# Optimization experiments

Hardware: AMD Instinct MI355X
Metric: run time of the kernel (lower is better)

The kernel has to match this reference:

```python
import jax, jax.numpy as jnp
import numpy as np

EMBED_DIM = 128
NUM_SYMBOLS = 200000
PAD_IDX = NUM_SYMBOLS
K_NEIGHBORS = 10
PROCESS_STEPS = 4
D_MODEL = 2 * EMBED_DIM   # 256
D_INNER = 2 * D_MODEL     # 512
LSTM_HID = 2 * D_MODEL    # 512
B, F_SUP, MAX_K = 4096, 5, 64


def setup_inputs() -> dict:
    key = jax.random.key(0)
    ks = jax.random.split(key, 40)
    f = lambda i, shape, s=0.05: jax.random.normal(ks[i], shape, jnp.float32) * s
    inp = {}
    inp['query'] = jax.random.randint(ks[0], (B, 2), 0, NUM_SYMBOLS)
    inp['support'] = jax.random.randint(ks[1], (F_SUP, 2), 0, NUM_SYMBOLS)
    inp['q_l1'] = jax.random.randint(ks[2], (B, MAX_K, 2), 0, NUM_SYMBOLS + 1)
    inp['q_deg_l'] = jax.random.randint(ks[3], (B,), 0, 100)
    inp['q_r1'] = jax.random.randint(ks[4], (B, MAX_K, 2), 0, NUM_SYMBOLS + 1)
    inp['q_deg_r'] = jax.random.randint(ks[5], (B,), 0, 100)
    inp['s_l1'] = jax.random.randint(ks[6], (F_SUP, MAX_K, 2), 0, NUM_SYMBOLS + 1)
    inp['s_deg_l'] = jax.random.randint(ks[7], (F_SUP,), 0, 100)
    inp['s_r1'] = jax.random.randint(ks[8], (F_SUP, MAX_K, 2), 0, NUM_SYMBOLS + 1)
    inp['s_deg_r'] = jax.random.randint(ks[9], (F_SUP,), 0, 100)
    # learned parameters
    inp['symbol_emb'] = f(10, (NUM_SYMBOLS + 1, EMBED_DIM), 0.1).at[PAD_IDX].set(0.0)
    inp['gcn_w_w'] = f(11, (EMBED_DIM, 2 * EMBED_DIM))
    inp['gcn_w_b'] = jnp.zeros((EMBED_DIM,), jnp.float32)
    inp['gcn_b'] = jnp.zeros((EMBED_DIM,), jnp.float32)
    inp['g1_w'] = f(12, (EMBED_DIM // 2, EMBED_DIM))
    inp['g1_b'] = jnp.zeros((EMBED_DIM // 2,), jnp.float32)
    inp['ln1_g'] = jnp.ones((EMBED_DIM // 2,), jnp.float32)
    inp['ln1_b'] = jnp.zeros((EMBED_DIM // 2,), jnp.float32)
    inp['g2_w'] = f(13, (1, EMBED_DIM // 2))
    inp['g2_b'] = jnp.zeros((1,), jnp.float32)
    inp['gate_temp'] = jnp.array(1.0, jnp.float32)
    inp['se_p1_w'] = f(14, (D_INNER, D_MODEL))
    inp['se_p1_b'] = jnp.zeros((D_INNER,), jnp.float32)
    inp['se_p2_w'] = f(15, (D_MODEL, D_INNER))
    inp['se_p2_b'] = jnp.zeros((D_MODEL,), jnp.float32)
    inp['se_ln_g'] = jnp.ones((D_MODEL,), jnp.float32)
    inp['se_ln_b'] = jnp.zeros((D_MODEL,), jnp.float32)
    inp['w_ih'] = f(16, (4 * LSTM_HID, D_MODEL))
    inp['w_hh'] = f(17, (4 * LSTM_HID, LSTM_HID))
    inp['b_ih'] = jnp.zeros((4 * LSTM_HID,), jnp.float32)
    inp['b_hh'] = jnp.zeros((4 * LSTM_HID,), jnp.float32)
    return inp


def _layernorm(x, g, b, eps=1e-5):
    m = jnp.mean(x, axis=-1, keepdims=True)
    v = jnp.var(x, axis=-1, keepdims=True)
    return (x - m) / jnp.sqrt(v + eps) * g + b


def _l2norm(x):
    return x / jnp.maximum(jnp.linalg.norm(x, axis=-1, keepdims=True), 1e-12)


def _neighbor_encoder(conn, deg, self_ids, p):
    emb = p['symbol_emb']
    rel, ent = conn[:, :, 0], conn[:, :, 1]
    rel_emb = emb[rel]            # [n, K, D] gather
    ent_emb = emb[ent]            # [n, K, D]
    self_emb = emb[self_ids]      # [n, D]
    sim = jnp.einsum('nd,nkd->nk', _l2norm(self_emb), _l2norm(ent_emb))
    is_pad = (rel == PAD_IDX).astype(jnp.float32)
    sim = sim - is_pad * 1e9
    k = min(K_NEIGHBORS, conn.shape[1])
    _, k_idx = jax.lax.top_k(sim, k)
    bidx = jnp.arange(conn.shape[0])[:, None]
    k_mask = jnp.zeros(sim.shape, jnp.float32).at[bidx, k_idx].set(1.0)[..., None]
    concat = jnp.concatenate([rel_emb, ent_emb], axis=-1)   # [n, K, 2D]
    proj = jax.nn.leaky_relu(concat @ p['gcn_w_w'].T + p['gcn_w_b'] + p['gcn_b'], 0.01)
    valid = (1.0 - is_pad[..., None]) * k_mask
    denom = jnp.maximum(jnp.sum(valid, axis=1), 1.0)
    agg = jnp.sum((proj * k_mask) * valid, axis=1) / denom   # [n, D]
    h = jax.nn.relu(_layernorm(agg @ p['g1_w'].T + p['g1_b'], p['ln1_g'], p['ln1_b']))
    logit = h @ p['g2_w'].T + p['g2_b']                      # [n, 1]
    temp = jnp.clip(p['gate_temp'], 0.1, 5.0)
    gate = jax.nn.sigmoid(logit / temp) * (deg > 0).astype(jnp.float32)[:, None]
    return jnp.tanh(self_emb + gate * agg)


def _support_encoder(x, p):
    h = jax.nn.relu(x @ p['se_p1_w'].T + p['se_p1_b'])
    h = h @ p['se_p2_w'].T + p['se_p2_b']
    return _layernorm(h + x, p['se_ln_g'], p['se_ln_b'])


def _query_encoder(support, query, p):
    n = query.shape[0]
    h_r0 = jnp.zeros((n, LSTM_HID), jnp.float32)
    c0 = jnp.zeros((n, LSTM_HID), jnp.float32)

    def step(carry, _):
        h_r, c = carry
        gates = query @ p['w_ih'].T + p['b_ih'] + h_r @ p['w_hh'].T + p['b_hh']
        i, f, g, o = jnp.split(gates, 4, axis=-1)
        c = jax.nn.sigmoid(f) * c + jax.nn.sigmoid(i) * jnp.tanh(g)
        h_ = jax.nn.sigmoid(o) * jnp.tanh(c)
        h = query + h_[:, :D_MODEL]
        attn = jax.nn.softmax(h @ support.T, axis=1)
        r = attn @ support
        return (jnp.concatenate([h, r], axis=-1), c), None

    (h_r, _), _ = jax.lax.scan(step, (h_r0, c0), None, length=PROCESS_STEPS)
    return h_r[:, :D_MODEL]


def reference(query, support, q_l1, q_deg_l, q_r1, q_deg_r, s_l1, s_deg_l, s_r1, s_deg_r,
              symbol_emb, gcn_w_w, gcn_w_b, gcn_b, g1_w, g1_b, ln1_g, ln1_b, g2_w, g2_b,
              gate_temp, se_p1_w, se_p1_b, se_p2_w, se_p2_b, se_ln_g, se_ln_b,
              w_ih, w_hh, b_ih, b_hh):
    p = dict(symbol_emb=symbol_emb, gcn_w_w=gcn_w_w, gcn_w_b=gcn_w_b, gcn_b=gcn_b,
             g1_w=g1_w, g1_b=g1_b, ln1_g=ln1_g, ln1_b=ln1_b, g2_w=g2_w, g2_b=g2_b,
             gate_temp=gate_temp, se_p1_w=se_p1_w, se_p1_b=se_p1_b, se_p2_w=se_p2_w,
             se_p2_b=se_p2_b, se_ln_g=se_ln_g, se_ln_b=se_ln_b,
             w_ih=w_ih, w_hh=w_hh, b_ih=b_ih, b_hh=b_hh)
    q_left = _neighbor_encoder(q_l1, q_deg_l, query[:, 0], p)
    q_right = _neighbor_encoder(q_r1, q_deg_r, query[:, 1], p)
    query_vec = jnp.concatenate([q_left, q_right], axis=-1)      # [B, 2D]
    s_left = _neighbor_encoder(s_l1, s_deg_l, support[:, 0], p)
    s_right = _neighbor_encoder(s_r1, s_deg_r, support[:, 1], p)
    support_vec = jnp.concatenate([s_left, s_right], axis=-1)    # [F, 2D]
    support_g = jnp.mean(_support_encoder(support_vec, p), axis=0, keepdims=True)  # [1, 2D]
    query_enc = _support_encoder(query_vec, p)                   # [B, 2D]
    query_g = _query_encoder(support_g, query_enc, p)            # [B, 2D]
    return jnp.sum(query_g * support_g, axis=1)                  # [B]
```

## Files before the change

kernel.cpp:

```cpp
#include <hip/hip_runtime.h>
#include <math.h>

#define BQ 4096
#define F_SUP 5
#define MAXK 64
#define ED 128
#define DM 256
#define DI 512
#define LH 512
#define NG 2048
#define PADX 200000
#define KNB 10
#define MROWS 82048
#define MREAL 82020
#define MQ 4224

typedef unsigned short u16;
typedef __attribute__((ext_vector_type(8))) short short8;
typedef __attribute__((ext_vector_type(4))) float floatx4;

__device__ __forceinline__ float sigf(float x) { return 1.0f / (1.0f + __expf(-x)); }
__device__ __forceinline__ float tanh_fast(float x) {
  float a = fabsf(x);
  float e = __expf(-2.0f * a);
  float t = (1.0f - e) / (1.0f + e);
  return copysignf(t, x);
}
__device__ __forceinline__ u16 f2bf(float f) {
  unsigned u = __float_as_uint(f);
  unsigned r = (u + 0x7FFFu + ((u >> 16) & 1u)) >> 16;
  return (u16)r;
}
__device__ __forceinline__ float bf2f(u16 u) {
  return __uint_as_float(((unsigned)u) << 16);
}
__device__ __forceinline__ void gl2lds16(const void* g, void* l) {
  __builtin_amdgcn_global_load_lds(
      (const __attribute__((address_space(1))) void*)g,
      (__attribute__((address_space(3))) void*)l, 16, 0, 0);
}

__global__ __launch_bounds__(256) void nbr_sim_kernel(
    const int* __restrict__ query, const int* __restrict__ support,
    const int* __restrict__ q_l1, const int* __restrict__ q_r1,
    const int* __restrict__ s_l1, const int* __restrict__ s_r1,
    const float* __restrict__ emb, float* __restrict__ simG)
{
  __shared__ __align__(16) float sE[128];
  int tid = threadIdx.x;
  int b = blockIdx.x;
  const int* conn; int self_id;
  if (b < BQ)              { int i = b;              conn = q_l1 + (long)i*(MAXK*2); self_id = query[2*i];   }
  else if (b < 2*BQ)       { int i = b - BQ;         conn = q_r1 + (long)i*(MAXK*2); self_id = query[2*i+1]; }
  else if (b < 2*BQ+F_SUP) { int i = b - 2*BQ;       conn = s_l1 + (long)i*(MAXK*2); self_id = support[2*i]; }
  else                     { int i = b - 2*BQ-F_SUP; conn = s_r1 + (long)i*(MAXK*2); self_id = support[2*i+1]; }

  int k = tid >> 2, part = tid & 3;
  int2 rc = *(const int2*)(conn + 2 * k);
  if (tid < 32) *(float4*)&sE[tid * 4] = *(const float4*)(emb + (long)self_id * ED + tid * 4);
  __syncthreads();

  const float* er = emb + (long)rc.y * ED + part * 4;
  float dot = 0.f, sq = 0.f;
  #pragma unroll
  for (int i = 0; i < 8; ++i) {
    float4 e = *(const float4*)(er + i * 16);
    float4 s = *(const float4*)(&sE[i * 16 + part * 4]);
    dot += e.x*s.x + e.y*s.y + e.z*s.z + e.w*s.w;
    sq  += e.x*e.x + e.y*e.y + e.z*e.z + e.w*e.w;
  }
  dot += __shfl_xor(dot, 1); dot += __shfl_xor(dot, 2);
  sq  += __shfl_xor(sq, 1);  sq  += __shfl_xor(sq, 2);
  if (part == 0) {
    float ne = fmaxf(sqrtf(sq), 1e-12f);
    float sim = dot / ne;
    if (rc.x == PADX) sim -= 1e9f;
    simG[(long)b * 64 + k] = sim;
  }
}

__global__ __launch_bounds__(256) void nbr_rank_kernel(
    const int* __restrict__ q_l1, const int* __restrict__ q_r1,
    const int* __restrict__ s_l1, const int* __restrict__ s_r1,
    const float* __restrict__ simG, int* __restrict__ idxA, int* __restrict__ meta)
{
  int tid = threadIdx.x;
  int wave = tid >> 6, lane = tid & 63;
  int b = blockIdx.x * 4 + wave;
  if (b < 2 * BQ + 2 * F_SUP) {
    const int* conn;
    if (b < BQ)              conn = q_l1 + (long)b * (MAXK*2);
    else if (b < 2*BQ)       conn = q_r1 + (long)(b - BQ) * (MAXK*2);
    else if (b < 2*BQ+F_SUP) conn = s_l1 + (long)(b - 2*BQ) * (MAXK*2);
    else                     conn = s_r1 + (long)(b - 2*BQ - F_SUP) * (MAXK*2);

    float my = simG[(long)b * 64 + lane];
    int rank = 0;
    #pragma unroll
    for (int j = 0; j < 64; ++j) {
      float s = __shfl(my, j);
      rank += ((s > my) || (s == my && j < lane)) ? 1 : 0;
    }
    int2 rc = *(const int2*)(conn + 2 * lane);
    bool val = (rank < KNB) && (rc.x != PADX);
    unsigned long long vm = __ballot(val ? 1 : 0);
    int cnt = __popcll(vm);
    long base = (long)b * 10;
    if (val) {
      int pos = __popcll(vm & ((1ull << lane) - 1ull));
      *(int2*)(idxA + (base + pos) * 2) = rc;
    }
    if (lane >= cnt && lane < KNB) {
      int2 pp; pp.x = PADX; pp.y = PADX;
      *(int2*)(idxA + (base + lane) * 2) = pp;
    }
    if (lane == 0) meta[b] = cnt;
  }
  if (blockIdx.x == 0 && tid < 2 * (MROWS - MREAL)) {
    idxA[(long)MREAL * 2 + tid] = PADX;
  }
}

__global__ __launch_bounds__(256) void proj_gather_gemm(
    const int* __restrict__ idxA, const float* __restrict__ emb,
    const u16* __restrict__ W, u16* __restrict__ proj)
{
  __shared__ u16 As[128 * 32];
  __shared__ u16 Bs[128 * 32];
  __shared__ int idxS[256];
  int tid = threadIdx.x;
  int bm = blockIdx.x;
  idxS[tid] = idxA[bm * 256 + tid];
  int lane = tid & 63, wave = tid >> 6;
  int wm = (wave & 1) * 64, wn = (wave >> 1) * 64;
  int col = lane & 15, quad = lane >> 4;
  int r = tid >> 1, part = tid & 1;

  floatx4 acc[4][4];
  #pragma unroll
  for (int i = 0; i < 4; ++i)
    #pragma unroll
    for (int j = 0; j < 4; ++j) { floatx4 z = {0.f,0.f,0.f,0.f}; acc[i][j] = z; }
  __syncthreads();

  for (int k0 = 0; k0 < 256; k0 += 32) {
    int half = k0 >> 7, koff = k0 & 127;
    #pragma unroll
    for (int t = 0; t < 2; ++t) {
      int c = t * 256 + tid;
      int rb = c >> 2, o = c & 3;
      int og = o ^ (rb & 3);
      gl2lds16(W + (long)rb * 256 + k0 + og * 8, &Bs[(size_t)c * 8]);
    }
    {
      int id = idxS[r * 2 + half];
      const float* src = emb + (long)id * ED + koff + part * 16;
      float4 f0 = *(const float4*)(src);
      float4 f1 = *(const float4*)(src + 4);
      float4 f2 = *(const float4*)(src + 8);
      float4 f3 = *(const float4*)(src + 12);
      short8 s0, s1;
      s0[0]=(short)f2bf(f0.x); s0[1]=(short)f2bf(f0.y); s0[2]=(short)f2bf(f0.z); s0[3]=(short)f2bf(f0.w);
      s0[4]=(short)f2bf(f1.x); s0[5]=(short)f2bf(f1.y); s0[6]=(short)f2bf(f1.z); s0[7]=(short)f2bf(f1.w);
      s1[0]=(short)f2bf(f2.x); s1[1]=(short)f2bf(f2.y); s1[2]=(short)f2bf(f2.z); s1[3]=(short)f2bf(f2.w);
      s1[4]=(short)f2bf(f3.x); s1[5]=(short)f2bf(f3.y); s1[6]=(short)f2bf(f3.z); s1[7]=(short)f2bf(f3.w);
      int o0 = 2 * part, o1 = 2 * part + 1;
      *(short8*)&As[(size_t)(r * 4 + (o0 ^ (r & 3))) * 8] = s0;
      *(short8*)&As[(size_t)(r * 4 + (o1 ^ (r & 3))) * 8] = s1;
    }
    __syncthreads();
    short8 af[4], bfr[4];
    #pragma unroll
    for (int i = 0; i < 4; ++i) {
      int ra = wm + i * 16 + col;
      af[i] = *(const short8*)&As[(size_t)(ra * 4 + (quad ^ (ra & 3))) * 8];
      int rb = wn + i * 16 + col;
      bfr[i] = *(const short8*)&Bs[(size_t)(rb * 4 + (quad ^ (rb & 3))) * 8];
    }
    #pragma unroll
    for (int i = 0; i < 4; ++i)
      #pragma unroll
      for (int j = 0; j < 4; ++j)
        acc[i][j] = __builtin_amdgcn_mfma_f32_16x16x32_bf16(af[i], bfr[j], acc[i][j], 0, 0, 0);
    __syncthreads();
  }
  int gm0 = bm * 128 + wm + quad * 4;
  int gn0 = wn + col;
  #pragma unroll
  for (int i = 0; i < 4; ++i)
    #pragma unroll
    for (int j = 0; j < 4; ++j)
      #pragma unroll
      for (int rr = 0; rr < 4; ++rr)
        proj[(long)(gm0 + i * 16 + rr) * 128 + gn0 + j * 16] = f2bf(acc[i][j][rr]);
}

__global__ __launch_bounds__(128) void nbr_post_kernel(
    const int* __restrict__ query, const int* __restrict__ support,
    const int* __restrict__ q_deg_l, const int* __restrict__ q_deg_r,
    const int* __restrict__ s_deg_l, const int* __restrict__ s_deg_r,
    const float* __restrict__ emb,
    const u16* __restrict__ proj, const int* __restrict__ meta,
    const float* __restrict__ gcn_w_b, const float* __restrict__ gcn_b,
    const float* __restrict__ g1_w, const float* __restrict__ g1_b,
    const float* __restrict__ ln1_g, const float* __restrict__ ln1_b,
    const float* __restrict__ g2_w, const float* __restrict__ g2_b,
    const float* __restrict__ gate_temp,
    float* __restrict__ qv, u16* __restrict__ qv_bf)
{
  __shared__ __align__(16) float aggS[128];
  __shared__ float sEs[128];
  __shared__ float gateS;
  int tid = threadIdx.x, b = blockIdx.x;
  int deg, self_id, row, colb;
  if (b < BQ)              { int i = b;              deg = q_deg_l[i]; self_id = query[2*i];     row = i;        colb = 0;  }
  else if (b < 2*BQ)       { int i = b - BQ;         deg = q_deg_r[i]; self_id = query[2*i+1];   row = i;        colb = ED; }
  else if (b < 2*BQ+F_SUP) { int i = b - 2*BQ;       deg = s_deg_l[i]; self_id = support[2*i];   row = BQ + i;   colb = 0;  }
  else                     { int i = b - 2*BQ-F_SUP; deg = s_deg_r[i]; self_id = support[2*i+1]; row = BQ + i;   colb = ED; }
  float* outp = qv + (long)row * DM + colb;
  u16*  outpb = qv_bf + (long)row * DM + colb;

  int cnt = meta[b];
  float denom = fmaxf((float)cnt, 1.0f);
  float bsum = gcn_w_b[tid] + gcn_b[tid];
  float agg = 0.f;
  long pbase = (long)b * 10;
  for (int kk = 0; kk < cnt; ++kk) {
    float z = bf2f(proj[(pbase + kk) * 128 + tid]) + bsum;
    z = (z >= 0.f) ? z : 0.01f * z;
    agg += z;
  }
  agg /= denom;
  aggS[tid] = agg;
  sEs[tid] = emb[(long)self_id * ED + tid];
  __syncthreads();

  if (tid < 64) {
    int e = tid;
    const float4* g1r = (const float4*)(g1_w + e * ED);
    float y = g1_b[e];
    #pragma unroll 8
    for (int j = 0; j < 32; ++j) {
      float4 w = g1r[j];
      float4 a = *(const float4*)&aggS[j * 4];
      y += w.x*a.x + w.y*a.y + w.z*a.z + w.w*a.w;
    }
    float s = y;
    #pragma unroll
    for (int off = 1; off < 64; off <<= 1) s += __shfl_xor(s, off);
    float mean = s * (1.0f / 64.0f);
    float dv = y - mean;
    float s2 = dv * dv;
    #pragma unroll
    for (int off = 1; off < 64; off <<= 1) s2 += __shfl_xor(s2, off);
    float var = s2 * (1.0f / 64.0f);
    float hv = dv / sqrtf(var + 1e-5f) * ln1_g[e] + ln1_b[e];
    hv = fmaxf(hv, 0.f);
    float lp = hv * g2_w[e];
    #pragma unroll
    for (int off = 1; off < 64; off <<= 1) lp += __shfl_xor(lp, off);
    if (e == 0) {
      float logit = lp + g2_b[0];
      float temp = fminf(fmaxf(gate_temp[0], 0.1f), 5.0f);
      float gate = 1.0f / (1.0f + expf(-logit / temp));
      if (deg <= 0) gate = 0.f;
      gateS = gate;
    }
  }
  __syncthreads();
  float o = tanhf(sEs[tid] + gateS * aggS[tid]);
  outp[tid] = o;
  outpb[tid] = f2bf(o);
}

__global__ __launch_bounds__(256) void mfma_gemm(
    const u16* __restrict__ A, int lda,
    const u16* __restrict__ W, int ldw,
    int N, int K,
    float* __restrict__ Cout, u16* __restrict__ Cbf,
    const float* __restrict__ bias0,
    const u16* __restrict__ gqin,
    u16* __restrict__ gqout,
    int relu, int lstm_mode,
    float* __restrict__ cstate, const float* __restrict__ qe,
    u16* __restrict__ hbf)
{
  __shared__ u16 As[128 * 32];
  __shared__ u16 Bs[128 * 32];
  int tid = threadIdx.x;
  int nb = N >> 7;
  int bn = blockIdx.x % nb, bm = blockIdx.x / nb;
  int lane = tid & 63, wave = tid >> 6;
  int wm = (wave & 1) * 64, wn = (wave >> 1) * 64;
  int col = lane & 15, quad = lane >> 4;

  u16 gqa[64]; float cpv[16]; float qev[16]; float scv[4];
  int u = 0; long fb = 0;
  if (lstm_mode) {
    u = bn * 32 + (wave >> 1) * 16 + col;
    fb = ((long)blockIdx.x * 4 + wave) * 64 + lane;
    #pragma unroll
    for (int j = 0; j < 4; ++j)
      scv[j] = bias0[bn * 128 + (wave >> 1) * 64 + j * 16 + col];
    if (lstm_mode == 1) {
      const short8* gp = (const short8*)(gqin + fb * 64);
      #pragma unroll
      for (int t = 0; t < 8; ++t) *(short8*)&gqa[t * 8] = gp[t];
      const float4* cp = (const float4*)(cstate + fb * 16);
      #pragma unroll
      for (int t = 0; t < 4; ++t) *(float4*)&cpv[t * 4] = cp[t];
    }
    if (u < DM) {
      #pragma unroll
      for (int i = 0; i < 4; ++i)
        #pragma unroll
        for (int r = 0; r < 4; ++r) {
          int m = bm * 128 + (wave & 1) * 64 + i * 16 + quad * 4 + r;
          qev[i * 4 + r] = qe[(long)m * DM + u];
        }
    }
  }

  floatx4 acc[4][4];
  #pragma unroll
  for (int i = 0; i < 4; ++i)
    #pragma unroll
    for (int j = 0; j < 4; ++j) { floatx4 z = {0.f,0.f,0.f,0.f}; acc[i][j] = z; }

  for (int k0 = 0; k0 < K; k0 += 32) {
    #pragma unroll
    for (int t = 0; t < 2; ++t) {
      int c = t * 256 + tid;
      int r = c >> 2, o = c & 3;
      int og = o ^ (r & 3);
      gl2lds16(A + (long)(bm * 128 + r) * lda + k0 + og * 8, &As[(size_t)c * 8]);
      gl2lds16(W + (long)(bn * 128 + r) * ldw + k0 + og * 8, &Bs[(size_t)c * 8]);
    }
    __syncthreads();
    short8 af[4], bfr[4];
    #pragma unroll
    for (int i = 0; i < 4; ++i) {
      int ra = wm + i * 16 + col;
      af[i] = *(const short8*)&As[(size_t)(ra * 4 + (quad ^ (ra & 3))) * 8];
      int rb = wn + i * 16 + col;
      bfr[i] = *(const short8*)&Bs[(size_t)(rb * 4 + (quad ^ (rb & 3))) * 8];
    }
    #pragma unroll
    for (int i = 0; i < 4; ++i)
      #pragma unroll
      for (int j = 0; j < 4; ++j)
        acc[i][j] = __builtin_amdgcn_mfma_f32_16x16x32_bf16(af[i], bfr[j], acc[i][j], 0, 0, 0);
    __syncthreads();
  }

  if (lstm_mode) {
    float cnew[16];
    #pragma unroll
    for (int i = 0; i < 4; ++i) {
      #pragma unroll
      for (int r = 0; r < 4; ++r) {
        float gI = acc[i][0][r] + scv[0];
        float gF = acc[i][1][r] + scv[1];
        float gG = acc[i][2][r] + scv[2];
        float gO = acc[i][3][r] + scv[3];
        if (lstm_mode == 1) {
          gI += bf2f(gqa[(i * 4 + 0) * 4 + r]);
          gF += bf2f(gqa[(i * 4 + 1) * 4 + r]);
          gG += bf2f(gqa[(i * 4 + 2) * 4 + r]);
          gO += bf2f(gqa[(i * 4 + 3) * 4 + r]);
        }
        float cp = (lstm_mode == 2) ? 0.f : cpv[i * 4 + r];
        float cn = sigf(gF) * cp + sigf(gI) * tanh_fast(gG);
        cnew[i * 4 + r] = cn;
        if (u < DM) {
          int m = bm * 128 + (wave & 1) * 64 + i * 16 + quad * 4 + r;
          hbf[(long)m * DM + u] = f2bf(qev[i * 4 + r] + sigf(gO) * tanh_fast(cn));
        }
      }
    }
    {
      float4* cp = (float4*)(cstate + fb * 16);
      #pragma unroll
      for (int t = 0; t < 4; ++t) cp[t] = *(float4*)&cnew[t * 4];
    }
    if (lstm_mode == 2) {
      u16 ga[64];
      #pragma unroll
      for (int i = 0; i < 4; ++i)
        #pragma unroll
        for (int j = 0; j < 4; ++j)
          #pragma unroll
          for (int r = 0; r < 4; ++r)
            ga[(i * 4 + j) * 4 + r] = f2bf(acc[i][j][r] + scv[j]);
      short8* gp = (short8*)(gqout + fb * 64);
      #pragma unroll
      for (int t = 0; t < 8; ++t) gp[t] = *(short8*)&ga[t * 8];
    }
  } else {
    int gm0 = bm * 128 + wm + quad * 4;
    int gn0 = bn * 128 + wn + col;
    #pragma unroll
    for (int i = 0; i < 4; ++i) {
      #pragma unroll
      for (int j = 0; j < 4; ++j) {
        int n = gn0 + j * 16;
        #pragma unroll
        for (int r = 0; r < 4; ++r) {
          int m = gm0 + i * 16 + r;
          float v = acc[i][j][r];
          if (bias0) v += bias0[n];
          if (relu) v = fmaxf(v, 0.f);
          if (Cout) Cout[(long)m * N + n] = v;
          if (Cbf)  Cbf[(long)m * N + n] = f2bf(v);
        }
      }
    }
  }
}

__global__ void prep_cast(
    const float* __restrict__ p1, const float* __restrict__ p2,
    const float* __restrict__ gcnw, const float* __restrict__ wih,
    const float* __restrict__ whh, const float* __restrict__ bih,
    const float* __restrict__ bhh,
    u16* __restrict__ p1b, u16* __restrict__ p2b, u16* __restrict__ gcnb,
    u16* __restrict__ wihb, u16* __restrict__ whhb, float* __restrict__ bihh)
{
  int gid = blockIdx.x * 256 + threadIdx.x;
  if (gid < 131072) { p1b[gid] = f2bf(p1[gid]); }
  else if (gid < 262144) { int i = gid - 131072; p2b[i] = f2bf(p2[i]); }
  else if (gid < 294912) { int i = gid - 262144; gcnb[i] = f2bf(gcnw[i]); }
  else if (gid < 819200) {
    int i = gid - 294912; int p = i >> 8, k = i & 255;
    int g = (p >> 4) & 3, uu = (p >> 7) * 32 + ((p >> 6) & 1) * 16 + (p & 15);
    int n = g * 512 + uu;
    wihb[i] = f2bf(wih[(long)n * DM + k]);
  } else if (gid < 1343488) {
    int i = gid - 819200; int p = i >> 8, k = i & 255;
    int g = (p >> 4) & 3, uu = (p >> 7) * 32 + ((p >> 6) & 1) * 16 + (p & 15);
    int n = g * 512 + uu;
    whhb[i] = f2bf(whh[(long)n * LH + k]);
  } else if (gid < 1345536) {
    int p = gid - 1343488;
    int g = (p >> 4) & 3, uu = (p >> 7) * 32 + ((p >> 6) & 1) * 16 + (p & 15);
    int n = g * 512 + uu;
    bihh[p] = bih[n] + bhh[n];
  }
}

__global__ __launch_bounds__(256) void ln_residual_kernel(
    const float* __restrict__ h2buf, const float* __restrict__ xbuf,
    const float* __restrict__ lng, const float* __restrict__ lnb,
    float* __restrict__ out, u16* __restrict__ outb)
{
  __shared__ float red[4];
  int r = blockIdx.x, tid = threadIdx.x;
  float v = h2buf[(long)r * DM + tid] + xbuf[(long)r * DM + tid];
  float s = v;
  #pragma unroll
  for (int off = 1; off < 64; off <<= 1) s += __shfl_xor(s, off);
  if ((tid & 63) == 0) red[tid >> 6] = s;
  __syncthreads();
  float mean = (red[0] + red[1] + red[2] + red[3]) * (1.0f / 256.0f);
  __syncthreads();
  float dv = v - mean;
  float s2 = dv * dv;
  #pragma unroll
  for (int off = 1; off < 64; off <<= 1) s2 += __shfl_xor(s2, off);
  if ((tid & 63) == 0) red[tid >> 6] = s2;
  __syncthreads();
  float var = (red[0] + red[1] + red[2] + red[3]) * (1.0f / 256.0f);
  float o = dv / sqrtf(var + 1e-5f) * lng[tid] + lnb[tid];
  out[(long)r * DM + tid] = o;
  outb[(long)r * DM + tid] = f2bf(o);
}

__global__ __launch_bounds__(256) void scorr_kernel(
    const float* __restrict__ qe, const float* __restrict__ whh,
    float* __restrict__ sg, float* __restrict__ s_corr_perm)
{
  __shared__ float sgS[DM];
  int tid = threadIdx.x;
  {
    float v = 0.f;
    #pragma unroll
    for (int r = 0; r < F_SUP; ++r) v += qe[(long)(BQ + r) * DM + tid];
    v *= (1.0f / (float)F_SUP);
    sgS[tid] = v;
    if (blockIdx.x == 0) sg[tid] = v;
  }
  __syncthreads();
  int wave = tid >> 6, lane = tid & 63;
  int n = blockIdx.x * 4 + wave;
  float4 w = *(const float4*)(whh + (long)n * LH + DM + lane * 4);
  float4 s = *(const float4*)&sgS[lane * 4];
  float d = w.x*s.x + w.y*s.y + w.z*s.z + w.w*s.w;
  #pragma unroll
  for (int off = 1; off < 64; off <<= 1) d += __shfl_xor(d, off);
  if (lane == 0) {
    int g = n >> 9, uu = n & 511;
    int p = (uu >> 5) * 128 + ((uu >> 4) & 1) * 64 + g * 16 + (uu & 15);
    s_corr_perm[p] = d;
  }
}

__global__ __launch_bounds__(256) void final_dot_kernel(
    const u16* __restrict__ h, const float* __restrict__ sg, float* __restrict__ out)
{
  __shared__ float red[4];
  int m = blockIdx.x, tid = threadIdx.x;
  float v = bf2f(h[(long)m * DM + tid]) * sg[tid];
  #pragma unroll
  for (int off = 1; off < 64; off <<= 1) v += __shfl_xor(v, off);
  if ((tid & 63) == 0) red[tid >> 6] = v;
  __syncthreads();
  if (tid == 0) out[m] = red[0] + red[1] + red[2] + red[3];
}

extern "C" void kernel_launch(void* const* d_in, const int* in_sizes, int n_in,
                              void* d_out, int out_size, void* d_ws, size_t ws_size,
                              hipStream_t stream)
{
  const int*   query    = (const int*)  d_in[0];
  const int*   support  = (const int*)  d_in[1];
  const int*   q_l1     = (const int*)  d_in[2];
  const int*   q_deg_l  = (const int*)  d_in[3];
  const int*   q_r1     = (const int*)  d_in[4];
  const int*   q_deg_r  = (const int*)  d_in[5];
  const int*   s_l1     = (const int*)  d_in[6];
  const int*   s_deg_l  = (const int*)  d_in[7];
  const int*   s_r1     = (const int*)  d_in[8];
  const int*   s_deg_r  = (const int*)  d_in[9];
  const float* symbol_emb = (const float*)d_in[10];
  const float* gcn_w_w  = (const float*)d_in[11];
  const float* gcn_w_b  = (const float*)d_in[12];
  const float* gcn_b    = (const float*)d_in[13];
  const float* g1_w     = (const float*)d_in[14];
  const float* g1_b     = (const float*)d_in[15];
  const float* ln1_g    = (const float*)d_in[16];
  const float* ln1_b    = (const float*)d_in[17];
  const float* g2_w     = (const float*)d_in[18];
  const float* g2_b     = (const float*)d_in[19];
  const float* gate_temp= (const float*)d_in[20];
  const float* se_p1_w  = (const float*)d_in[21];
  const float* se_p1_b  = (const float*)d_in[22];
  const float* se_p2_w  = (const float*)d_in[23];
  const float* se_p2_b  = (const float*)d_in[24];
  const float* se_ln_g  = (const float*)d_in[25];
  const float* se_ln_b  = (const float*)d_in[26];
  const float* w_ih     = (const float*)d_in[27];
  const float* w_hh     = (const float*)d_in[28];
  const float* b_ih     = (const float*)d_in[29];
  const float* b_hh     = (const float*)d_in[30];

  float* ws = (float*)d_ws;
  size_t off = 0;
  float* projF   = ws + off; off += (size_t)MROWS * 128 / 2;
  float* idxF    = ws + off; off += (size_t)MROWS * 2;
  float* qv      = ws + off; off += (size_t)MQ * DM;
  float* qe      = ws + off; off += (size_t)MQ * DM;
  float* qv_bfF  = ws + off; off += (size_t)MQ * DM / 2;
  float* qe_bfF  = ws + off; off += (size_t)MQ * DM / 2;
  float* h1bF    = ws + off; off += (size_t)MQ * DI / 2;
  float* H2      = ws + off; off += (size_t)MQ * DM;
  float* gqbF    = ws + off; off += (size_t)BQ * NG / 2;
  float* cstate  = ws + off; off += (size_t)BQ * LH;
  float* hbf0F   = ws + off; off += (size_t)BQ * DM / 2;
  float* hbf1F   = ws + off; off += (size_t)BQ * DM / 2;
  float* p1bF    = ws + off; off += 131072 / 2;
  float* p2bF    = ws + off; off += 131072 / 2;
  float* gcnbF   = ws + off; off += 32768 / 2;
  float* wihbF   = ws + off; off += 524288 / 2;
  float* whhbF   = ws + off; off += 524288 / 2;
  float* bihh    = ws + off; off += 2048;
  float* sg      = ws + off; off += 256;
  float* s_corr  = ws + off; off += 2048;
  float* metaF   = ws + off; off += 8448;
  float* simF    = ws + off; off += (size_t)8448 * 64;

  u16* proj   = (u16*)projF;
  int* idxA   = (int*)idxF;
  u16* qv_bf  = (u16*)qv_bfF;
  u16* qe_bf  = (u16*)qe_bfF;
  u16* H1_bf  = (u16*)h1bF;
  u16* gq_fr  = (u16*)gqbF;
  u16* hbf0   = (u16*)hbf0F;
  u16* hbf1   = (u16*)hbf1F;
  u16* p1b    = (u16*)p1bF;
  u16* p2b    = (u16*)p2bF;
  u16* gcnb   = (u16*)gcnbF;
  u16* wihb   = (u16*)wihbF;
  u16* whhb   = (u16*)whhbF;
  int* meta   = (int*)metaF;

  prep_cast<<<5256, 256, 0, stream>>>(se_p1_w, se_p2_w, gcn_w_w, w_ih, w_hh, b_ih, b_hh,
                                      p1b, p2b, gcnb, wihb, whhb, bihh);

  nbr_sim_kernel<<<2 * BQ + 2 * F_SUP, 256, 0, stream>>>(
      query, support, q_l1, q_r1, s_l1, s_r1, symbol_emb, simF);

  nbr_rank_kernel<<<(2 * BQ + 2 * F_SUP + 3) / 4, 256, 0, stream>>>(
      q_l1, q_r1, s_l1, s_r1, simF, idxA, meta);

  proj_gather_gemm<<<MROWS / 128, 256, 0, stream>>>(idxA, symbol_emb, gcnb, proj);

  nbr_post_kernel<<<2 * BQ + 2 * F_SUP, 128, 0, stream>>>(
      query, support, q_deg_l, q_deg_r, s_deg_l, s_deg_r, symbol_emb,
      proj, meta, gcn_w_b, gcn_b, g1_w, g1_b, ln1_g, ln1_b, g2_w, g2_b, gate_temp,
      qv, qv_bf);

  mfma_gemm<<<(MQ / 128) * (DI / 128), 256, 0, stream>>>(qv_bf, 256, p1b, 256, DI, 256,
      nullptr, H1_bf, se_p1_b, nullptr, nullptr, 1, 0, nullptr, nullptr, nullptr);
  mfma_gemm<<<(MQ / 128) * (DM / 128), 256, 0, stream>>>(H1_bf, 512, p2b, 512, DM, 512,
      H2, nullptr, se_p2_b, nullptr, nullptr, 0, 0, nullptr, nullptr, nullptr);
  ln_residual_kernel<<<BQ + F_SUP, 256, 0, stream>>>(H2, qv, se_ln_g, se_ln_b, qe, qe_bf);

  scorr_kernel<<<512, 256, 0, stream>>>(qe, w_hh, sg, s_corr);

  mfma_gemm<<<(BQ / 128) * (NG / 128), 256, 0, stream>>>(qe_bf, 256, wihb, 256, NG, 256,
      nullptr, nullptr, bihh, nullptr, gq_fr, 0, 2, cstate, qe, hbf0);

  mfma_gemm<<<(BQ / 128) * (NG / 128), 256, 0, stream>>>(hbf0, 256, whhb, 256, NG, 256,
      nullptr, nullptr, s_corr, gq_fr, nullptr, 0, 1, cstate, qe, hbf1);
  mfma_gemm<<<(BQ / 128) * (NG / 128), 256, 0, stream>>>(hbf1, 256, whhb, 256, NG, 256,
      nullptr, nullptr, s_corr, gq_fr, nullptr, 0, 1, cstate, qe, hbf0);
  mfma_gemm<<<(BQ / 128) * (NG / 128), 256, 0, stream>>>(hbf0, 256, whhb, 256, NG, 256,
      nullptr, nullptr, s_corr, gq_fr, nullptr, 0, 1, cstate, qe, hbf1);

  final_dot_kernel<<<BQ, 256, 0, stream>>>(hbf1, sg, (float*)d_out);
}
```

Measured before the change: 428.1 us.

## Pre-cast embedding table to bf16, fuse sim and rank, gather via LDS loads

Adds a pass that converts the whole embedding table to bf16 each call. The neighbor-similarity and top-k ranking kernels now read the halved-size rows and are merged into one kernel, with ranking done through shared memory. The projection GEMM gathers bf16 embedding rows directly into LDS with global_load_lds instead of converting in registers. The aim is to halve random gather traffic and drop a launch plus an intermediate buffer, at the cost of a full-table cast pass and bf16 similarity scores that may alter top-k tie-breaking.

```diff
diff --git a/kernel.cpp b/kernel.cpp
--- a/kernel.cpp
+++ b/kernel.cpp
@@ -14,6 +14,7 @@
 #define MROWS 82048
 #define MREAL 82020
 #define MQ 4224
+#define EMB_ELEMS 25600128
 
 typedef unsigned short u16;
 typedef __attribute__((ext_vector_type(8))) short short8;
@@ -40,13 +41,28 @@
       (__attribute__((address_space(3))) void*)l, 16, 0, 0);
 }
 
-__global__ __launch_bounds__(256) void nbr_sim_kernel(
+__global__ __launch_bounds__(256) void emb_cast_kernel(
+    const float* __restrict__ emb, u16* __restrict__ embb)
+{
+  long i = ((long)blockIdx.x * 256 + threadIdx.x) * 8;
+  if (i >= (long)EMB_ELEMS) return;
+  float4 f0 = *(const float4*)(emb + i);
+  float4 f1 = *(const float4*)(emb + i + 4);
+  short8 s;
+  s[0]=(short)f2bf(f0.x); s[1]=(short)f2bf(f0.y); s[2]=(short)f2bf(f0.z); s[3]=(short)f2bf(f0.w);
+  s[4]=(short)f2bf(f1.x); s[5]=(short)f2bf(f1.y); s[6]=(short)f2bf(f1.z); s[7]=(short)f2bf(f1.w);
+  *(short8*)(embb + i) = s;
+}
+
+__global__ __launch_bounds__(256) void nbr_simrank_kernel(
     const int* __restrict__ query, const int* __restrict__ support,
     const int* __restrict__ q_l1, const int* __restrict__ q_r1,
     const int* __restrict__ s_l1, const int* __restrict__ s_r1,
-    const float* __restrict__ emb, float* __restrict__ simG)
-{
-  __shared__ __align__(16) float sE[128];
+    const u16* __restrict__ embb, int* __restrict__ idxA, int* __restrict__ meta)
+{
+  __shared__ float sE[128];
+  __shared__ float simS[64];
+  __shared__ int relS[64], entS[64];
   int tid = threadIdx.x;
   int b = blockIdx.x;
   const int* conn; int self_id;
@@ -57,17 +73,24 @@
 
   int k = tid >> 2, part = tid & 3;
   int2 rc = *(const int2*)(conn + 2 * k);
-  if (tid < 32) *(float4*)&sE[tid * 4] = *(const float4*)(emb + (long)self_id * ED + tid * 4);
-  __syncthreads();
-
-  const float* er = emb + (long)rc.y * ED + part * 4;
+  if (tid < 16) {
+    short8 s = *(const short8*)(embb + (long)self_id * ED + tid * 8);
+    #pragma unroll
+    for (int j = 0; j < 8; ++j) sE[tid * 8 + j] = bf2f((u16)s[j]);
+  }
+  __syncthreads();
+
+  const u16* er = embb + (long)rc.y * ED + part * 8;
   float dot = 0.f, sq = 0.f;
   #pragma unroll
-  for (int i = 0; i < 8; ++i) {
-    float4 e = *(const float4*)(er + i * 16);
-    float4 s = *(const float4*)(&sE[i * 16 + part * 4]);
-    dot += e.x*s.x + e.y*s.y + e.z*s.z + e.w*s.w;
-    sq  += e.x*e.x + e.y*e.y + e.z*e.z + e.w*e.w;
+  for (int i = 0; i < 4; ++i) {
+    short8 e8 = *(const short8*)(er + i * 32);
+    #pragma unroll
+    for (int j = 0; j < 8; ++j) {
+      float e = bf2f((u16)e8[j]);
+      float s = sE[i * 32 + part * 8 + j];
+      dot += e * s; sq += e * e;
+    }
   }
   dot += __shfl_xor(dot, 1); dot += __shfl_xor(dot, 2);
   sq  += __shfl_xor(sq, 1);  sq  += __shfl_xor(sq, 2);
@@ -75,54 +98,40 @@
     float ne = fmaxf(sqrtf(sq), 1e-12f);
     float sim = dot / ne;
     if (rc.x == PADX) sim -= 1e9f;
-    simG[(long)b * 64 + k] = sim;
-  }
-}
-
-__global__ __launch_bounds__(256) void nbr_rank_kernel(
-    const int* __restrict__ q_l1, const int* __restrict__ q_r1,
-    const int* __restrict__ s_l1, const int* __restrict__ s_r1,
-    const float* __restrict__ simG, int* __restrict__ idxA, int* __restrict__ meta)
-{
-  int tid = threadIdx.x;
-  int wave = tid >> 6, lane = tid & 63;
-  int b = blockIdx.x * 4 + wave;
-  if (b < 2 * BQ + 2 * F_SUP) {
-    const int* conn;
-    if (b < BQ)              conn = q_l1 + (long)b * (MAXK*2);
-    else if (b < 2*BQ)       conn = q_r1 + (long)(b - BQ) * (MAXK*2);
-    else if (b < 2*BQ+F_SUP) conn = s_l1 + (long)(b - 2*BQ) * (MAXK*2);
-    else                     conn = s_r1 + (long)(b - 2*BQ - F_SUP) * (MAXK*2);
-
-    float my = simG[(long)b * 64 + lane];
+    simS[k] = sim; relS[k] = rc.x; entS[k] = rc.y;
+  }
+  __syncthreads();
+
+  if (tid < 64) {
+    float my = simS[tid];
     int rank = 0;
     #pragma unroll
     for (int j = 0; j < 64; ++j) {
-      float s = __shfl(my, j);
-      rank += ((s > my) || (s == my && j < lane)) ? 1 : 0;
-    }
-    int2 rc = *(const int2*)(conn + 2 * lane);
-    bool val = (rank < KNB) && (rc.x != PADX);
+      float s = simS[j];
+      rank += ((s > my) || (s == my && j < tid)) ? 1 : 0;
+    }
+    bool val = (rank < KNB) && (relS[tid] != PADX);
     unsigned long long vm = __ballot(val ? 1 : 0);
     int cnt = __popcll(vm);
     long base = (long)b * 10;
     if (val) {
-      int pos = __popcll(vm & ((1ull << lane) - 1ull));
-      *(int2*)(idxA + (base + pos) * 2) = rc;
-    }
-    if (lane >= cnt && lane < KNB) {
+      int pos = __popcll(vm & ((1ull << tid) - 1ull));
+      int2 p; p.x = relS[tid]; p.y = entS[tid];
+      *(int2*)(idxA + (base + pos) * 2) = p;
+    }
+    if (tid >= cnt && tid < KNB) {
       int2 pp; pp.x = PADX; pp.y = PADX;
-      *(int2*)(idxA + (base + lane) * 2) = pp;
-    }
-    if (lane == 0) meta[b] = cnt;
-  }
-  if (blockIdx.x == 0 && tid < 2 * (MROWS - MREAL)) {
-    idxA[(long)MREAL * 2 + tid] = PADX;
+      *(int2*)(idxA + (base + tid) * 2) = pp;
+    }
+    if (tid == 0) meta[b] = cnt;
+  }
+  if (b == 0 && tid >= 64 && tid < 64 + 2 * (MROWS - MREAL)) {
+    idxA[(long)MREAL * 2 + (tid - 64)] = PADX;
   }
 }
 
 __global__ __launch_bounds__(256) void proj_gather_gemm(
-    const int* __restrict__ idxA, const float* __restrict__ emb,
+    const int* __restrict__ idxA, const u16* __restrict__ embb,
     const u16* __restrict__ W, u16* __restrict__ proj)
 {
   __shared__ u16 As[128 * 32];
@@ -134,7 +143,6 @@
   int lane = tid & 63, wave = tid >> 6;
   int wm = (wave & 1) * 64, wn = (wave >> 1) * 64;
   int col = lane & 15, quad = lane >> 4;
-  int r = tid >> 1, part = tid & 1;
 
   floatx4 acc[4][4];
   #pragma unroll
@@ -151,22 +159,8 @@
       int rb = c >> 2, o = c & 3;
       int og = o ^ (rb & 3);
       gl2lds16(W + (long)rb * 256 + k0 + og * 8, &Bs[(size_t)c * 8]);
-    }
-    {
-      int id = idxS[r * 2 + half];
-      const float* src = emb + (long)id * ED + koff + part * 16;
-      float4 f0 = *(const float4*)(src);
-      float4 f1 = *(const float4*)(src + 4);
-      float4 f2 = *(const float4*)(src + 8);
-      float4 f3 = *(const float4*)(src + 12);
-      short8 s0, s1;
-      s0[0]=(short)f2bf(f0.x); s0[1]=(short)f2bf(f0.y); s0[2]=(short)f2bf(f0.z); s0[3]=(short)f2bf(f0.w);
-      s0[4]=(short)f2bf(f1.x); s0[5]=(short)f2bf(f1.y); s0[6]=(short)f2bf(f1.z); s0[7]=(short)f2bf(f1.w);
-      s1[0]=(short)f2bf(f2.x); s1[1]=(short)f2bf(f2.y); s1[2]=(short)f2bf(f2.z); s1[3]=(short)f2bf(f2.w);
-      s1[4]=(short)f2bf(f3.x); s1[5]=(short)f2bf(f3.y); s1[6]=(short)f2bf(f3.z); s1[7]=(short)f2bf(f3.w);
-      int o0 = 2 * part, o1 = 2 * part + 1;
-      *(short8*)&As[(size_t)(r * 4 + (o0 ^ (r & 3))) * 8] = s0;
-      *(short8*)&As[(size_t)(r * 4 + (o1 ^ (r & 3))) * 8] = s1;
+      int id = idxS[rb * 2 + half];
+      gl2lds16(embb + (long)id * ED + koff + og * 8, &As[(size_t)c * 8]);
     }
     __syncthreads();
     short8 af[4], bfr[4];
@@ -576,7 +570,7 @@
   float* sg      = ws + off; off += 256;
   float* s_corr  = ws + off; off += 2048;
   float* metaF   = ws + off; off += 8448;
-  float* simF    = ws + off; off += (size_t)8448 * 64;
+  float* embbF   = ws + off; off += (size_t)EMB_ELEMS / 2;
 
   u16* proj   = (u16*)projF;
   int* idxA   = (int*)idxF;
@@ -592,17 +586,16 @@
   u16* wihb   = (u16*)wihbF;
   u16* whhb   = (u16*)whhbF;
   int* meta   = (int*)metaF;
+  u16* embb   = (u16*)embbF;
 
   prep_cast<<<5256, 256, 0, stream>>>(se_p1_w, se_p2_w, gcn_w_w, w_ih, w_hh, b_ih, b_hh,
                                       p1b, p2b, gcnb, wihb, whhb, bihh);
-
-  nbr_sim_kernel<<<2 * BQ + 2 * F_SUP, 256, 0, stream>>>(
-      query, support, q_l1, q_r1, s_l1, s_r1, symbol_emb, simF);
-
-  nbr_rank_kernel<<<(2 * BQ + 2 * F_SUP + 3) / 4, 256, 0, stream>>>(
-      q_l1, q_r1, s_l1, s_r1, simF, idxA, meta);
-
-  proj_gather_gemm<<<MROWS / 128, 256, 0, stream>>>(idxA, symbol_emb, gcnb, proj);
+  emb_cast_kernel<<<(EMB_ELEMS / 8 + 255) / 256, 256, 0, stream>>>(symbol_emb, embb);
+
+  nbr_simrank_kernel<<<2 * BQ + 2 * F_SUP, 256, 0, stream>>>(
+      query, support, q_l1, q_r1, s_l1, s_r1, embb, idxA, meta);
+
+  proj_gather_gemm<<<MROWS / 128, 256, 0, stream>>>(idxA, embb, gcnb, proj);
 
   nbr_post_kernel<<<2 * BQ + 2 * F_SUP, 128, 0, stream>>>(
       query, support, q_deg_l, q_deg_r, s_deg_l, s_deg_r, symbol_emb,
```

After: 426.5 us. About the same (-0.4%).
